# Performance work log

Hardware: AMD Instinct MI355X
Metric: run time of the kernel (lower is better)

## Reference

```python
import jax, jax.numpy as jnp
import numpy as np

N_NODES = 100000
N_EDGES = 1600000
NUM_GRAPHS = 64
D = 128      # num_node_features
H = 256      # hidden_dim
OUT = 1      # output_dim
GA = 6       # num_graph_attributes


def setup_inputs() -> dict:
    key = jax.random.key(0)
    ks = jax.random.split(key, 20)
    p = lambda k, shape: (jax.random.normal(k, shape, jnp.float32) * 0.02)
    return {
        "x": jax.random.normal(ks[0], (N_NODES, D), jnp.float32),
        "edge_index": jax.random.randint(ks[1], (2, N_EDGES), 0, N_NODES),
        "batch": jnp.sort(jax.random.randint(ks[2], (N_NODES,), 0, NUM_GRAPHS)),
        "graph_attr": jax.random.normal(ks[3], (NUM_GRAPHS, GA), jnp.float32),
        # conv1 MLP: Linear(D->H), ReLU, Linear(H->H)
        "w1a": p(ks[4], (D, H)), "b1a": p(ks[5], (H,)),
        "w1b": p(ks[6], (H, H)), "b1b": p(ks[7], (H,)),
        # conv2 MLP: Linear(H->H), ReLU, Linear(H->H)
        "w2a": p(ks[8], (H, H)), "b2a": p(ks[9], (H,)),
        "w2b": p(ks[10], (H, H)), "b2b": p(ks[11], (H,)),
        # head
        "wf1": p(ks[12], (H + GA, H)), "bf1": p(ks[13], (H,)),
        "wf2": p(ks[14], (H, OUT)), "bf2": p(ks[15], (OUT,)),
    }


def _gin_conv(x, src, dst, wa, ba, wb, bb):
    # GINConv with default eps=0: MLP((1+0)*x_i + sum_{j->i} x_j)
    agg = jax.ops.segment_sum(x[src], dst, num_segments=N_NODES)  # [N, d]
    h = x + agg
    h = jax.nn.relu(h @ wa + ba)
    return h @ wb + bb


def reference(x, edge_index, batch, graph_attr,
              w1a, b1a, w1b, b1b, w2a, b2a, w2b, b2b,
              wf1, bf1, wf2, bf2):
    src, dst = edge_index[0], edge_index[1]
    h = jax.nn.relu(_gin_conv(x, src, dst, w1a, b1a, w1b, b1b))  # [N, H]
    h = _gin_conv(h, src, dst, w2a, b2a, w2b, b2b)               # [N, H]
    # global mean pool per graph
    sums = jax.ops.segment_sum(h, batch, num_segments=NUM_GRAPHS)          # [G, H]
    cnts = jax.ops.segment_sum(jnp.ones((h.shape[0], 1), h.dtype), batch,
                               num_segments=NUM_GRAPHS)                    # [G, 1]
    pooled = sums / jnp.maximum(cnts, 1.0)
    g = jnp.concatenate([pooled, graph_attr.reshape(-1, GA)], axis=1)      # [G, H+GA]
    g = jax.nn.relu(g @ wf1 + bf1)
    return g @ wf2 + bf2                                                   # [G, OUT]
```

## Files before the change

### kernel.cpp

```cpp
#include <hip/hip_runtime.h>

#define N_NODES 100000
#define N_EDGES 1600000
#define NGRAPH  64
#define DIN     128
#define HID     256
#define GA      6

#define NBUCK  98
#define BSHIFT 10
#define BCAP   20480

typedef __attribute__((ext_vector_type(8))) short bf16x8;
typedef __attribute__((ext_vector_type(4))) float f32x4;

__device__ __forceinline__ unsigned short f2bf(float f) {
  unsigned int u = __float_as_uint(f);
  u += 0x7fffu + ((u >> 16) & 1u);
  return (unsigned short)(u >> 16);
}
__device__ __forceinline__ float bf_lo(unsigned int u) { return __uint_as_float(u << 16); }
__device__ __forceinline__ float bf_hi(unsigned int u) { return __uint_as_float(u & 0xffff0000u); }
__device__ __forceinline__ unsigned int packbf(float lo, float hi) {
  return (unsigned int)f2bf(lo) | ((unsigned int)f2bf(hi) << 16);
}

__device__ __forceinline__ void gload16(const void* g, void* l) {
  __builtin_amdgcn_global_load_lds(
      (const __attribute__((address_space(1))) unsigned int*)g,
      (__attribute__((address_space(3))) unsigned int*)l, 16, 0, 0);
}


__global__ __launch_bounds__(256) void cvt_all(const float* __restrict__ x,
                                               const float* __restrict__ w1a,
                                               const float* __restrict__ w1b,
                                               const float* __restrict__ w2a,
                                               const float* __restrict__ w2b,
                                               unsigned short* __restrict__ xo,
                                               unsigned short* __restrict__ o1a,
                                               unsigned short* __restrict__ o1b,
                                               unsigned short* __restrict__ o2a,
                                               unsigned short* __restrict__ o2b) {
  int bid = blockIdx.x, tid = threadIdx.x;
  if (bid < 12500) {
    size_t idx = ((size_t)bid * 256 + tid) * 4;
    float4 v = *(const float4*)&x[idx];
    ushort4 o;
    o.x = f2bf(v.x); o.y = f2bf(v.y); o.z = f2bf(v.z); o.w = f2bf(v.w);
    *(ushort4*)&xo[idx] = o;
    return;
  }
  bid -= 12500;
  const float* in; unsigned short* out; int shift, idx;
  if (bid < 128)      { in = w1a; out = o1a; shift = 7; idx = bid * 256 + tid; }
  else if (bid < 384) { in = w1b; out = o1b; shift = 8; idx = (bid - 128) * 256 + tid; }
  else if (bid < 640) { in = w2a; out = o2a; shift = 8; idx = (bid - 384) * 256 + tid; }
  else                { in = w2b; out = o2b; shift = 8; idx = (bid - 640) * 256 + tid; }
  int K = 1 << shift;
  int n = idx >> shift;
  int k = idx & (K - 1);
  out[idx] = f2bf(in[(size_t)k * HID + n]);
}


__global__ __launch_bounds__(256) void bin_kernel(const int* __restrict__ esrc,
                                                  const int* __restrict__ edst,
                                                  int* __restrict__ cursor,
                                                  unsigned int* __restrict__ tmp) {
  __shared__ unsigned int pk[4096];
  __shared__ unsigned char bkb[4096];
  __shared__ int hist[NBUCK], lbase[NBUCK + 1], gbase[NBUCK], lcur[NBUCK];
  const int tid = threadIdx.x;
  const int lane = tid & 63;
  const int ebase = blockIdx.x * 4096;
  const int n = min(4096, N_EDGES - ebase);
  if (tid < NBUCK) hist[tid] = 0;
  __syncthreads();
  unsigned int pkv[16]; int bk[16];
#pragma unroll
  for (int i = 0; i < 16; i++) {
    int e = ebase + i * 256 + tid;
    bk[i] = -1;
    if (e < N_EDGES) {
      int s = esrc[e], d = edst[e];
      bk[i] = d >> BSHIFT;
      pkv[i] = (unsigned int)s | ((unsigned int)(d & ((1 << BSHIFT) - 1)) << 17);
      atomicAdd(&hist[bk[i]], 1);
    }
  }
  __syncthreads();
  if (tid < 64) {
    int i0 = 2 * tid, i1 = i0 + 1;
    int a0 = (i0 < NBUCK) ? hist[i0] : 0;
    int a1 = (i1 < NBUCK) ? hist[i1] : 0;
    int p = a0 + a1, sc = p;
#pragma unroll
    for (int off = 1; off < 64; off <<= 1) {
      int t = __shfl_up(sc, off);
      if (lane >= off) sc += t;
    }
    int excl = sc - p;
    if (i0 < NBUCK) lbase[i0] = excl;
    if (i1 < NBUCK) lbase[i1] = excl + a0;
    if (tid == 63) lbase[NBUCK] = sc;
  }
  __syncthreads();
  if (tid < NBUCK) {
    int c = hist[tid];
    gbase[tid] = c ? atomicAdd(&cursor[tid], c) : 0;
    lcur[tid] = lbase[tid];
  }
  __syncthreads();
#pragma unroll
  for (int i = 0; i < 16; i++) {
    if (bk[i] >= 0) {
      int pos = atomicAdd(&lcur[bk[i]], 1);
      pk[pos] = pkv[i];
      bkb[pos] = (unsigned char)bk[i];
    }
  }
  __syncthreads();
#pragma unroll
  for (int i = 0; i < 16; i++) {
    int idx = i * 256 + tid;
    if (idx < n) {
      int b = bkb[idx];
      tmp[(size_t)b * BCAP + gbase[b] + (idx - lbase[b])] = pk[idx];
    }
  }
}


__global__ __launch_bounds__(512) void sort_kernel(const unsigned int* __restrict__ tmp,
                                                   const int* __restrict__ cnt,
                                                   int* __restrict__ csr,
                                                   int* __restrict__ ssrc) {
  __shared__ int nhist[1024], ncur[1024];
  __shared__ int bb[NBUCK];
  __shared__ int wsum[8];
  const int b = blockIdx.x;
  const int tid = threadIdx.x;
  const int lane = tid & 63, wid = tid >> 6;
  if (tid < 64) {
    int i0 = 2 * tid, i1 = i0 + 1;
    int a0 = (i0 < NBUCK) ? cnt[i0] : 0;
    int a1 = (i1 < NBUCK) ? cnt[i1] : 0;
    int p = a0 + a1, sc = p;
#pragma unroll
    for (int off = 1; off < 64; off <<= 1) {
      int t = __shfl_up(sc, off);
      if (lane >= off) sc += t;
    }
    int excl = sc - p;
    if (i0 < NBUCK) bb[i0] = excl;
    if (i1 < NBUCK) bb[i1] = excl + a0;
  }
  nhist[tid] = 0; nhist[tid + 512] = 0;
  __syncthreads();
  const int myCnt = cnt[b];
  const int ebase = bb[b];
  const unsigned int* srcp = tmp + (size_t)b * BCAP;
  for (int i = tid; i < myCnt; i += 512)
    atomicAdd(&nhist[srcp[i] >> 17], 1);
  __syncthreads();
  int i0 = 2 * tid;
  int a0 = nhist[i0], a1 = nhist[i0 + 1];
  int p = a0 + a1, sc = p;
#pragma unroll
  for (int off = 1; off < 64; off <<= 1) {
    int t = __shfl_up(sc, off);
    if (lane >= off) sc += t;
  }
  if (lane == 63) wsum[wid] = sc;
  __syncthreads();
  if (tid < 8) {
    int ws = wsum[tid];
#pragma unroll
    for (int off = 1; off < 8; off <<= 1) {
      int t = __shfl_up(ws, off);
      if (tid >= off) ws += t;
    }
    wsum[tid] = ws;
  }
  __syncthreads();
  int excl = ((wid > 0) ? wsum[wid - 1] : 0) + sc - p;
  ncur[i0] = excl;
  ncur[i0 + 1] = excl + a0;
  int node0 = (b << BSHIFT) + i0;
  if (node0 < N_NODES) csr[node0] = ebase + excl;
  if (node0 + 1 < N_NODES) csr[node0 + 1] = ebase + excl + a0;
  if (b == 0 && tid == 0) csr[N_NODES] = N_EDGES;
  __syncthreads();
  for (int i = tid; i < myCnt; i += 512) {
    unsigned int pe = srcp[i];
    int pos = atomicAdd(&ncur[pe >> 17], 1);
    ssrc[ebase + pos] = (int)(pe & 0x1FFFF);
  }
}


__global__ __launch_bounds__(256) void agg1_kernel(const uint2* __restrict__ x,
                                                   const int* __restrict__ csr,
                                                   const int* __restrict__ ssrc,
                                                   uint2* __restrict__ out,
                                                   int base) {
  int node = base + blockIdx.x * 4 + (threadIdx.x >> 6);
  int lane = threadIdx.x & 63;
  int half = lane >> 5;
  int dl   = lane & 31;
  float a0 = 0.f, a1 = 0.f, a2 = 0.f, a3 = 0.f;
  if (half == 0) {
    uint2 u = x[(size_t)node * 32 + dl];
    a0 = bf_lo(u.x); a1 = bf_hi(u.x); a2 = bf_lo(u.y); a3 = bf_hi(u.y);
  }
  int s = csr[node], e = csr[node + 1];
  int i = s;
  for (; i + 8 <= e; i += 8) {
    int s0 = ssrc[i + half],     s1 = ssrc[i + 2 + half];
    int s2 = ssrc[i + 4 + half], s3 = ssrc[i + 6 + half];
    uint2 v0 = x[(size_t)s0 * 32 + dl];
    uint2 v1 = x[(size_t)s1 * 32 + dl];
    uint2 v2 = x[(size_t)s2 * 32 + dl];
    uint2 v3 = x[(size_t)s3 * 32 + dl];
    a0 += bf_lo(v0.x) + bf_lo(v1.x) + bf_lo(v2.x) + bf_lo(v3.x);
    a1 += bf_hi(v0.x) + bf_hi(v1.x) + bf_hi(v2.x) + bf_hi(v3.x);
    a2 += bf_lo(v0.y) + bf_lo(v1.y) + bf_lo(v2.y) + bf_lo(v3.y);
    a3 += bf_hi(v0.y) + bf_hi(v1.y) + bf_hi(v2.y) + bf_hi(v3.y);
  }
  for (; i + 2 <= e; i += 2) {
    int sn = ssrc[i + half];
    uint2 v = x[(size_t)sn * 32 + dl];
    a0 += bf_lo(v.x); a1 += bf_hi(v.x);
    a2 += bf_lo(v.y); a3 += bf_hi(v.y);
  }
  if (i < e && half == 0) {
    uint2 v = x[(size_t)ssrc[i] * 32 + dl];
    a0 += bf_lo(v.x); a1 += bf_hi(v.x);
    a2 += bf_lo(v.y); a3 += bf_hi(v.y);
  }
  a0 += __shfl_xor(a0, 32);
  a1 += __shfl_xor(a1, 32);
  a2 += __shfl_xor(a2, 32);
  a3 += __shfl_xor(a3, 32);
  if (half == 0) {
    uint2 o;
    o.x = packbf(a0, a1);
    o.y = packbf(a2, a3);
    out[(size_t)node * 32 + dl] = o;
  }
}

__global__ __launch_bounds__(256) void agg2_kernel(const uint2* __restrict__ x,
                                                   const int* __restrict__ csr,
                                                   const int* __restrict__ ssrc,
                                                   uint2* __restrict__ out,
                                                   int base) {
  int node = base + blockIdx.x * 4 + (threadIdx.x >> 6);
  int lane = threadIdx.x & 63;
  uint2 u = x[(size_t)node * 64 + lane];
  float a0 = bf_lo(u.x), a1 = bf_hi(u.x), a2 = bf_lo(u.y), a3 = bf_hi(u.y);
  int s = csr[node], e = csr[node + 1];
  int i = s;
  for (; i + 8 <= e; i += 8) {
    int n0 = ssrc[i],     n1 = ssrc[i + 1], n2 = ssrc[i + 2], n3 = ssrc[i + 3];
    int n4 = ssrc[i + 4], n5 = ssrc[i + 5], n6 = ssrc[i + 6], n7 = ssrc[i + 7];
    uint2 v0 = x[(size_t)n0 * 64 + lane];
    uint2 v1 = x[(size_t)n1 * 64 + lane];
    uint2 v2 = x[(size_t)n2 * 64 + lane];
    uint2 v3 = x[(size_t)n3 * 64 + lane];
    uint2 v4 = x[(size_t)n4 * 64 + lane];
    uint2 v5 = x[(size_t)n5 * 64 + lane];
    uint2 v6 = x[(size_t)n6 * 64 + lane];
    uint2 v7 = x[(size_t)n7 * 64 + lane];
    a0 += (bf_lo(v0.x) + bf_lo(v1.x)) + (bf_lo(v2.x) + bf_lo(v3.x)) +
          (bf_lo(v4.x) + bf_lo(v5.x)) + (bf_lo(v6.x) + bf_lo(v7.x));
    a1 += (bf_hi(v0.x) + bf_hi(v1.x)) + (bf_hi(v2.x) + bf_hi(v3.x)) +
          (bf_hi(v4.x) + bf_hi(v5.x)) + (bf_hi(v6.x) + bf_hi(v7.x));
    a2 += (bf_lo(v0.y) + bf_lo(v1.y)) + (bf_lo(v2.y) + bf_lo(v3.y)) +
          (bf_lo(v4.y) + bf_lo(v5.y)) + (bf_lo(v6.y) + bf_lo(v7.y));
    a3 += (bf_hi(v0.y) + bf_hi(v1.y)) + (bf_hi(v2.y) + bf_hi(v3.y)) +
          (bf_hi(v4.y) + bf_hi(v5.y)) + (bf_hi(v6.y) + bf_hi(v7.y));
  }
  for (; i < e; i++) {
    uint2 v = x[(size_t)ssrc[i] * 64 + lane];
    a0 += bf_lo(v.x); a1 += bf_hi(v.x);
    a2 += bf_lo(v.y); a3 += bf_hi(v.y);
  }
  uint2 o;
  o.x = packbf(a0, a1);
  o.y = packbf(a2, a3);
  out[(size_t)node * 64 + lane] = o;
}


template<int K, bool RELU>
__global__ __launch_bounds__(256, 4)
void gemm128(const unsigned short* __restrict__ A,
             const unsigned short* __restrict__ Wt,
             const float* __restrict__ bias,
             unsigned short* __restrict__ C) {
  __shared__ unsigned short Asl[128 * 64];
  __shared__ unsigned short Wsl[128 * 64];
  const int tid = threadIdx.x;
  const int lane = tid & 63;
  const int w = tid >> 6;
  const int wm = w >> 1, wn = w & 1;
  const int l15 = lane & 15, l4 = lane >> 4, l7 = lane & 7;
  const int rowBase = (blockIdx.x >> 1) * 128;
  const int colBase = (blockIdx.x & 1) * 128;

  f32x4 acc[4][4] = {};

  for (int k0 = 0; k0 < K; k0 += 64) {
#pragma unroll
    for (int i = 0; i < 4; i++) {
      int c = i * 256 + tid;
      int m = c >> 3, koL = c & 7;
      int koS = koL ^ (m & 7);
      int gr = rowBase + m; if (gr >= N_NODES) gr = N_NODES - 1;
      gload16(&A[(size_t)gr * K + k0 + koS * 8], Asl + (size_t)c * 8);
    }
#pragma unroll
    for (int i = 0; i < 4; i++) {
      int c = i * 256 + tid;
      int n = c >> 3, koL = c & 7;
      int koS = koL ^ (n & 7);
      gload16(&Wt[(size_t)(colBase + n) * K + k0 + koS * 8], Wsl + (size_t)c * 8);
    }
    __syncthreads();
#pragma unroll
    for (int kk = 0; kk < 2; kk++) {
      int koX = (kk * 4 + l4) ^ l7;
      bf16x8 a[4], b[4];
#pragma unroll
      for (int f = 0; f < 4; f++) {
        int rowA = wm * 64 + f * 16 + l15;
        int rowB = wn * 64 + f * 16 + l15;
        a[f] = *(const bf16x8*)&Asl[(size_t)(rowA * 64 + koX * 8)];
        b[f] = *(const bf16x8*)&Wsl[(size_t)(rowB * 64 + koX * 8)];
      }
#pragma unroll
      for (int fm = 0; fm < 4; fm++)
#pragma unroll
        for (int fn = 0; fn < 4; fn++)
          acc[fm][fn] = __builtin_amdgcn_mfma_f32_16x16x32_bf16(a[fm], b[fn], acc[fm][fn], 0, 0, 0);
    }
    __syncthreads();
  }

#pragma unroll
  for (int fm = 0; fm < 4; fm++) {
    int r0 = rowBase + wm * 64 + fm * 16 + l4 * 4;
#pragma unroll
    for (int fn = 0; fn < 4; fn++) {
      int col = colBase + wn * 64 + fn * 16 + l15;
      float bb = bias[col];
#pragma unroll
      for (int j = 0; j < 4; j++) {
        int r = r0 + j;
        if (r < N_NODES) {
          float v = acc[fm][fn][j] + bb;
          if (RELU) v = fmaxf(v, 0.f);
          C[(size_t)r * HID + col] = f2bf(v);
        }
      }
    }
  }
}


__global__ __launch_bounds__(256) void pool_kernel(const unsigned short* __restrict__ H,
                                                   const int* __restrict__ batch,
                                                   float* __restrict__ sums,
                                                   float* __restrict__ cnts) {
  int d = threadIdx.x;
  int n0 = blockIdx.x * 128;
  int n1 = n0 + 128; if (n1 > N_NODES) n1 = N_NODES;
  int cur = batch[n0];
  float run = 0.f, runc = 0.f;
  for (int i = n0; i < n1; i++) {
    int b = batch[i];
    if (b != cur) {
      atomicAdd(&sums[(size_t)cur * HID + d], run);
      if (d == 0) atomicAdd(&cnts[cur], runc);
      run = 0.f; runc = 0.f; cur = b;
    }
    run += __uint_as_float(((unsigned int)H[(size_t)i * HID + d]) << 16);
    runc += 1.f;
  }
  atomicAdd(&sums[(size_t)cur * HID + d], run);
  if (d == 0) atomicAdd(&cnts[cur], runc);
}


__global__ __launch_bounds__(256) void head_kernel(const float* __restrict__ sums,
                                                   const float* __restrict__ cnts,
                                                   const float* __restrict__ gattr,
                                                   const float* __restrict__ wf1,
                                                   const float* __restrict__ bf1,
                                                   const float* __restrict__ wf2,
                                                   const float* __restrict__ bf2,
                                                   float* __restrict__ out) {
  int g = blockIdx.x, tid = threadIdx.x;
  __shared__ float gv[HID + GA + 2];
  __shared__ float red[256];
  float c = cnts[g]; c = fmaxf(c, 1.0f);
  gv[tid] = sums[(size_t)g * HID + tid] / c;
  if (tid < GA) gv[HID + tid] = gattr[g * GA + tid];
  if (tid < 2) gv[HID + GA + tid] = 0.f;
  __syncthreads();
  float ac0 = 0.f, ac1 = 0.f, ac2 = 0.f, ac3 = 0.f;
  float ac4 = 0.f, ac5 = 0.f, ac6 = 0.f, ac7 = 0.f;
  const float* wcol = wf1 + tid;
  int k = 0;
#pragma unroll 1
  for (; k + 8 <= HID + GA; k += 8) {
    float w0 = wcol[(size_t)(k + 0) * HID];
    float w1 = wcol[(size_t)(k + 1) * HID];
    float w2 = wcol[(size_t)(k + 2) * HID];
    float w3 = wcol[(size_t)(k + 3) * HID];
    float w4 = wcol[(size_t)(k + 4) * HID];
    float w5 = wcol[(size_t)(k + 5) * HID];
    float w6 = wcol[(size_t)(k + 6) * HID];
    float w7 = wcol[(size_t)(k + 7) * HID];
    ac0 = fmaf(gv[k + 0], w0, ac0);
    ac1 = fmaf(gv[k + 1], w1, ac1);
    ac2 = fmaf(gv[k + 2], w2, ac2);
    ac3 = fmaf(gv[k + 3], w3, ac3);
    ac4 = fmaf(gv[k + 4], w4, ac4);
    ac5 = fmaf(gv[k + 5], w5, ac5);
    ac6 = fmaf(gv[k + 6], w6, ac6);
    ac7 = fmaf(gv[k + 7], w7, ac7);
  }
  for (; k < HID + GA; k++)
    ac0 = fmaf(gv[k], wcol[(size_t)k * HID], ac0);
  float acc = ((ac0 + ac1) + (ac2 + ac3)) + ((ac4 + ac5) + (ac6 + ac7)) + bf1[tid];
  float h = fmaxf(acc, 0.f);
  red[tid] = h * wf2[tid];
  __syncthreads();
  for (int s = 128; s > 0; s >>= 1) {
    if (tid < s) red[tid] += red[tid + s];
    __syncthreads();
  }
  if (tid == 0) out[g] = red[0] + bf2[0];
}


extern "C" void kernel_launch(void* const* d_in, const int* in_sizes, int n_in,
                              void* d_out, int out_size, void* d_ws, size_t ws_size,
                              hipStream_t stream) {
  const float* x     = (const float*)d_in[0];
  const int*   eidx  = (const int*)d_in[1];
  const int*   batch = (const int*)d_in[2];
  const float* gattr = (const float*)d_in[3];
  const float* w1a = (const float*)d_in[4];  const float* b1a = (const float*)d_in[5];
  const float* w1b = (const float*)d_in[6];  const float* b1b = (const float*)d_in[7];
  const float* w2a = (const float*)d_in[8];  const float* b2a = (const float*)d_in[9];
  const float* w2b = (const float*)d_in[10]; const float* b2b = (const float*)d_in[11];
  const float* wf1 = (const float*)d_in[12]; const float* bf1 = (const float*)d_in[13];
  const float* wf2 = (const float*)d_in[14]; const float* bf2 = (const float*)d_in[15];
  float* out = (float*)d_out;

  const int* esrc = eidx;
  const int* edst = eidx + N_EDGES;

  char* w = (char*)d_ws;
  auto alloc = [&](size_t bytes) -> void* {
    void* p = (void*)w;
    w += (bytes + 255) & ~(size_t)255;
    return p;
  };
  unsigned short* B0 = (unsigned short*)alloc((size_t)N_NODES * DIN * 2);
  unsigned short* B1 = (unsigned short*)alloc((size_t)N_NODES * HID * 2);
  unsigned short* B2 = (unsigned short*)alloc((size_t)N_NODES * HID * 2);
  unsigned short* B3 = (unsigned short*)alloc((size_t)N_NODES * HID * 2);
  unsigned short* w1aT = (unsigned short*)alloc(256 * 128 * 2);
  unsigned short* w1bT = (unsigned short*)alloc(256 * 256 * 2);
  unsigned short* w2aT = (unsigned short*)alloc(256 * 256 * 2);
  unsigned short* w2bT = (unsigned short*)alloc(256 * 256 * 2);
  int*   csr    = (int*)alloc((N_NODES + 4) * 4);
  int*   cursor = (int*)alloc(NBUCK * 4);
  unsigned int* tmp = (unsigned int*)alloc((size_t)NBUCK * BCAP * 4);
  int*   ssrc   = (int*)alloc((size_t)N_EDGES * 4);
  float* sums   = (float*)alloc((size_t)NGRAPH * HID * 4);
  float* cnts   = (float*)alloc(NGRAPH * 4);

  hipMemsetAsync(cursor, 0, NBUCK * 4, stream);
  hipMemsetAsync(sums, 0, (size_t)NGRAPH * HID * 4 + 256, stream);

  cvt_all<<<12500 + 896, 256, 0, stream>>>(x, w1a, w1b, w2a, w2b,
                                           B0, w1aT, w1bT, w2aT, w2bT);

  bin_kernel<<<(N_EDGES + 4095) / 4096, 256, 0, stream>>>(esrc, edst, cursor, tmp);
  sort_kernel<<<NBUCK, 512, 0, stream>>>(tmp, cursor, csr, ssrc);

  const int ngemm = ((N_NODES + 127) / 128) * 2;
  const int half = N_NODES / 2;

  agg1_kernel<<<half / 4, 256, 0, stream>>>((const uint2*)B0, csr, ssrc, (uint2*)B1, 0);
  agg1_kernel<<<half / 4, 256, 0, stream>>>((const uint2*)B0, csr, ssrc, (uint2*)B1, half);
  gemm128<128, true><<<ngemm, 256, 0, stream>>>(B1, w1aT, b1a, B3);
  gemm128<256, true><<<ngemm, 256, 0, stream>>>(B3, w1bT, b1b, B2);
  agg2_kernel<<<half / 4, 256, 0, stream>>>((const uint2*)B2, csr, ssrc, (uint2*)B1, 0);
  agg2_kernel<<<half / 4, 256, 0, stream>>>((const uint2*)B2, csr, ssrc, (uint2*)B1, half);
  gemm128<256, true><<<ngemm, 256, 0, stream>>>(B1, w2aT, b2a, B3);
  gemm128<256, false><<<ngemm, 256, 0, stream>>>(B3, w2bT, b2b, B2);

  pool_kernel<<<(N_NODES + 127) / 128, 256, 0, stream>>>(B2, batch, sums, cnts);
  head_kernel<<<NGRAPH, 256, 0, stream>>>(sums, cnts, gattr, wf1, bf1, wf2, bf2, out);
}
```

Measured before the change: 438.8 us.

## Widen GEMM tile to full 256 columns, split edge buckets finer, merge aggregation launches

The GEMM now uses 512-thread blocks that compute a 128x256 tile covering all output columns. Each A tile is loaded once per block instead of twice across two column blocks. The edge bucketing switches to 512-node buckets (196 buckets), which gives the sort kernel more blocks and one node per thread in its scan. The split agg launches are merged into single launches. The larger GEMM block uses more LDS and registers per block, which could limit occupancy.

Measured after the change: 949.3 us. 116% more time.

```diff
diff --git a/kernel.cpp b/kernel.cpp
--- a/kernel.cpp
+++ b/kernel.cpp
@@ -7,9 +7,9 @@
 #define HID     256
 #define GA      6
 
-#define NBUCK  98
-#define BSHIFT 10
-#define BCAP   20480
+#define NBUCK  196
+#define BSHIFT 9
+#define BCAP   10240
 
 typedef __attribute__((ext_vector_type(8))) short bf16x8;
 typedef __attribute__((ext_vector_type(4))) float f32x4;
@@ -91,18 +91,22 @@
   }
   __syncthreads();
   if (tid < 64) {
-    int i0 = 2 * tid, i1 = i0 + 1;
-    int a0 = (i0 < NBUCK) ? hist[i0] : 0;
-    int a1 = (i1 < NBUCK) ? hist[i1] : 0;
-    int p = a0 + a1, sc = p;
+    int i0 = 4 * tid;
+    int a0 = (i0 + 0 < NBUCK) ? hist[i0 + 0] : 0;
+    int a1 = (i0 + 1 < NBUCK) ? hist[i0 + 1] : 0;
+    int a2 = (i0 + 2 < NBUCK) ? hist[i0 + 2] : 0;
+    int a3 = (i0 + 3 < NBUCK) ? hist[i0 + 3] : 0;
+    int p = a0 + a1 + a2 + a3, sc = p;
 #pragma unroll
     for (int off = 1; off < 64; off <<= 1) {
       int t = __shfl_up(sc, off);
       if (lane >= off) sc += t;
     }
     int excl = sc - p;
-    if (i0 < NBUCK) lbase[i0] = excl;
-    if (i1 < NBUCK) lbase[i1] = excl + a0;
+    if (i0 + 0 < NBUCK) lbase[i0 + 0] = excl;
+    if (i0 + 1 < NBUCK) lbase[i0 + 1] = excl + a0;
+    if (i0 + 2 < NBUCK) lbase[i0 + 2] = excl + a0 + a1;
+    if (i0 + 3 < NBUCK) lbase[i0 + 3] = excl + a0 + a1 + a2;
     if (tid == 63) lbase[NBUCK] = sc;
   }
   __syncthreads();
@@ -136,27 +140,31 @@
                                                    const int* __restrict__ cnt,
                                                    int* __restrict__ csr,
                                                    int* __restrict__ ssrc) {
-  __shared__ int nhist[1024], ncur[1024];
+  __shared__ int nhist[512], ncur[512];
   __shared__ int bb[NBUCK];
   __shared__ int wsum[8];
   const int b = blockIdx.x;
   const int tid = threadIdx.x;
   const int lane = tid & 63, wid = tid >> 6;
   if (tid < 64) {
-    int i0 = 2 * tid, i1 = i0 + 1;
-    int a0 = (i0 < NBUCK) ? cnt[i0] : 0;
-    int a1 = (i1 < NBUCK) ? cnt[i1] : 0;
-    int p = a0 + a1, sc = p;
+    int i0 = 4 * tid;
+    int a0 = (i0 + 0 < NBUCK) ? cnt[i0 + 0] : 0;
+    int a1 = (i0 + 1 < NBUCK) ? cnt[i0 + 1] : 0;
+    int a2 = (i0 + 2 < NBUCK) ? cnt[i0 + 2] : 0;
+    int a3 = (i0 + 3 < NBUCK) ? cnt[i0 + 3] : 0;
+    int p = a0 + a1 + a2 + a3, sc = p;
 #pragma unroll
     for (int off = 1; off < 64; off <<= 1) {
       int t = __shfl_up(sc, off);
       if (lane >= off) sc += t;
     }
     int excl = sc - p;
-    if (i0 < NBUCK) bb[i0] = excl;
-    if (i1 < NBUCK) bb[i1] = excl + a0;
-  }
-  nhist[tid] = 0; nhist[tid + 512] = 0;
+    if (i0 + 0 < NBUCK) bb[i0 + 0] = excl;
+    if (i0 + 1 < NBUCK) bb[i0 + 1] = excl + a0;
+    if (i0 + 2 < NBUCK) bb[i0 + 2] = excl + a0 + a1;
+    if (i0 + 3 < NBUCK) bb[i0 + 3] = excl + a0 + a1 + a2;
+  }
+  nhist[tid] = 0;
   __syncthreads();
   const int myCnt = cnt[b];
   const int ebase = bb[b];
@@ -164,9 +172,8 @@
   for (int i = tid; i < myCnt; i += 512)
     atomicAdd(&nhist[srcp[i] >> 17], 1);
   __syncthreads();
-  int i0 = 2 * tid;
-  int a0 = nhist[i0], a1 = nhist[i0 + 1];
-  int p = a0 + a1, sc = p;
+  int v = nhist[tid];
+  int sc = v;
 #pragma unroll
   for (int off = 1; off < 64; off <<= 1) {
     int t = __shfl_up(sc, off);
@@ -184,12 +191,10 @@
     wsum[tid] = ws;
   }
   __syncthreads();
-  int excl = ((wid > 0) ? wsum[wid - 1] : 0) + sc - p;
-  ncur[i0] = excl;
-  ncur[i0 + 1] = excl + a0;
-  int node0 = (b << BSHIFT) + i0;
+  int excl = ((wid > 0) ? wsum[wid - 1] : 0) + sc - v;
+  ncur[tid] = excl;
+  int node0 = (b << BSHIFT) + tid;
   if (node0 < N_NODES) csr[node0] = ebase + excl;
-  if (node0 + 1 < N_NODES) csr[node0 + 1] = ebase + excl + a0;
   if (b == 0 && tid == 0) csr[N_NODES] = N_EDGES;
   __syncthreads();
   for (int i = tid; i < myCnt; i += 512) {
@@ -203,9 +208,8 @@
 __global__ __launch_bounds__(256) void agg1_kernel(const uint2* __restrict__ x,
                                                    const int* __restrict__ csr,
                                                    const int* __restrict__ ssrc,
-                                                   uint2* __restrict__ out,
-                                                   int base) {
-  int node = base + blockIdx.x * 4 + (threadIdx.x >> 6);
+                                                   uint2* __restrict__ out) {
+  int node = blockIdx.x * 4 + (threadIdx.x >> 6);
   int lane = threadIdx.x & 63;
   int half = lane >> 5;
   int dl   = lane & 31;
@@ -254,9 +258,8 @@
 __global__ __launch_bounds__(256) void agg2_kernel(const uint2* __restrict__ x,
                                                    const int* __restrict__ csr,
                                                    const int* __restrict__ ssrc,
-                                                   uint2* __restrict__ out,
-                                                   int base) {
-  int node = base + blockIdx.x * 4 + (threadIdx.x >> 6);
+                                                   uint2* __restrict__ out) {
+  int node = blockIdx.x * 4 + (threadIdx.x >> 6);
   int lane = threadIdx.x & 63;
   uint2 u = x[(size_t)node * 64 + lane];
   float a0 = bf_lo(u.x), a1 = bf_hi(u.x), a2 = bf_lo(u.y), a3 = bf_hi(u.y);
@@ -295,27 +298,27 @@
 
 
 template<int K, bool RELU>
-__global__ __launch_bounds__(256, 4)
+__global__ __launch_bounds__(512, 6)
 void gemm128(const unsigned short* __restrict__ A,
              const unsigned short* __restrict__ Wt,
              const float* __restrict__ bias,
              unsigned short* __restrict__ C) {
   __shared__ unsigned short Asl[128 * 64];
-  __shared__ unsigned short Wsl[128 * 64];
+  __shared__ unsigned short Wsl[256 * 64];
   const int tid = threadIdx.x;
   const int lane = tid & 63;
   const int w = tid >> 6;
-  const int wm = w >> 1, wn = w & 1;
+  const int wm = w >> 2;
+  const int wn = w & 3;
   const int l15 = lane & 15, l4 = lane >> 4, l7 = lane & 7;
-  const int rowBase = (blockIdx.x >> 1) * 128;
-  const int colBase = (blockIdx.x & 1) * 128;
+  const int rowBase = blockIdx.x * 128;
 
   f32x4 acc[4][4] = {};
 
   for (int k0 = 0; k0 < K; k0 += 64) {
 #pragma unroll
-    for (int i = 0; i < 4; i++) {
-      int c = i * 256 + tid;
+    for (int i = 0; i < 2; i++) {
+      int c = i * 512 + tid;
       int m = c >> 3, koL = c & 7;
       int koS = koL ^ (m & 7);
       int gr = rowBase + m; if (gr >= N_NODES) gr = N_NODES - 1;
@@ -323,10 +326,10 @@
     }
 #pragma unroll
     for (int i = 0; i < 4; i++) {
-      int c = i * 256 + tid;
+      int c = i * 512 + tid;
       int n = c >> 3, koL = c & 7;
       int koS = koL ^ (n & 7);
-      gload16(&Wt[(size_t)(colBase + n) * K + k0 + koS * 8], Wsl + (size_t)c * 8);
+      gload16(&Wt[(size_t)n * K + k0 + koS * 8], Wsl + (size_t)c * 8);
     }
     __syncthreads();
 #pragma unroll
@@ -354,7 +357,7 @@
     int r0 = rowBase + wm * 64 + fm * 16 + l4 * 4;
 #pragma unroll
     for (int fn = 0; fn < 4; fn++) {
-      int col = colBase + wn * 64 + fn * 16 + l15;
+      int col = wn * 64 + fn * 16 + l15;
       float bb = bias[col];
 #pragma unroll
       for (int j = 0; j < 4; j++) {
@@ -495,17 +498,14 @@
   bin_kernel<<<(N_EDGES + 4095) / 4096, 256, 0, stream>>>(esrc, edst, cursor, tmp);
   sort_kernel<<<NBUCK, 512, 0, stream>>>(tmp, cursor, csr, ssrc);
 
-  const int ngemm = ((N_NODES + 127) / 128) * 2;
-  const int half = N_NODES / 2;
-
-  agg1_kernel<<<half / 4, 256, 0, stream>>>((const uint2*)B0, csr, ssrc, (uint2*)B1, 0);
-  agg1_kernel<<<half / 4, 256, 0, stream>>>((const uint2*)B0, csr, ssrc, (uint2*)B1, half);
-  gemm128<128, true><<<ngemm, 256, 0, stream>>>(B1, w1aT, b1a, B3);
-  gemm128<256, true><<<ngemm, 256, 0, stream>>>(B3, w1bT, b1b, B2);
-  agg2_kernel<<<half / 4, 256, 0, stream>>>((const uint2*)B2, csr, ssrc, (uint2*)B1, 0);
-  agg2_kernel<<<half / 4, 256, 0, stream>>>((const uint2*)B2, csr, ssrc, (uint2*)B1, half);
-  gemm128<256, true><<<ngemm, 256, 0, stream>>>(B1, w2aT, b2a, B3);
-  gemm128<256, false><<<ngemm, 256, 0, stream>>>(B3, w2bT, b2b, B2);
+  const int ngemm = (N_NODES + 127) / 128;
+
+  agg1_kernel<<<N_NODES / 4, 256, 0, stream>>>((const uint2*)B0, csr, ssrc, (uint2*)B1);
+  gemm128<128, true><<<ngemm, 512, 0, stream>>>(B1, w1aT, b1a, B3);
+  gemm128<256, true><<<ngemm, 512, 0, stream>>>(B3, w1bT, b1b, B2);
+  agg2_kernel<<<N_NODES / 4, 256, 0, stream>>>((const uint2*)B2, csr, ssrc, (uint2*)B1);
+  gemm128<256, true><<<ngemm, 512, 0, stream>>>(B1, w2aT, b2a, B3);
+  gemm128<256, false><<<ngemm, 512, 0, stream>>>(B3, w2bT, b2b, B2);
 
   pool_kernel<<<(N_NODES + 127) / 128, 256, 0, stream>>>(B2, batch, sums, cnts);
   head_kernel<<<NGRAPH, 256, 0, stream>>>(sums, cnts, gattr, wf1, bf1, wf2, bf2, out);
```
